# Optimization experiments

Hardware: AMD Instinct MI355X
Metric: run time of the kernel (lower is better)

## Reference

```python
import jax, jax.numpy as jnp
import numpy as np

NUM_CLASSES = 6
HIERARCHY_WEIGHT = 0.2


def _build_class_weights():
    w = np.ones(NUM_CLASSES, dtype=np.float32)
    w[0] = 1.2; w[1] = 1.0; w[2] = 1.1; w[3] = 1.3; w[4] = 1.0; w[5] = 1.1
    return jnp.asarray(w)


def _build_hierarchy_matrix():
    p = np.ones((NUM_CLASSES, NUM_CLASSES), dtype=np.float32)
    p[2, 3] = 0.5; p[3, 2] = 0.5
    p[0, 4] = 0.6; p[4, 0] = 0.6
    p[1, 5] = 0.7; p[5, 1] = 0.7
    p[0, 1] = 1.5; p[1, 0] = 1.5
    p[2, 5] = 1.4; p[5, 2] = 1.4
    return jnp.asarray(p)


def setup_inputs() -> dict:
    key = jax.random.key(0)
    k1, k2 = jax.random.split(key)
    B = 4194304
    predictions = jax.random.normal(k1, (B, NUM_CLASSES), dtype=jnp.float32)
    targets = jax.random.randint(k2, (B,), 0, NUM_CLASSES, dtype=jnp.int64)
    return {
        "predictions": predictions,
        "targets": targets,
        "class_weights": _build_class_weights(),
        "hierarchy_matrix": _build_hierarchy_matrix(),
    }


def reference(predictions, targets, class_weights, hierarchy_matrix):
    B = predictions.shape[0]
    # Weighted cross-entropy, matching torch's weighted-mean reduction:
    # sum_i w[t_i] * nll_i / sum_i w[t_i]
    logp = jax.nn.log_softmax(predictions, axis=-1)            # (B, C)
    nll = -jnp.take_along_axis(logp, targets[:, None], axis=-1)[:, 0]  # (B,)
    w = class_weights[targets]                                  # (B,)
    ce_loss = jnp.sum(w * nll) / jnp.sum(w)

    # Hierarchy penalty: sum_{i, j != t_i} probs[i,j] * penalty[t_i, j] / B
    probs = jax.nn.softmax(predictions, axis=-1)               # (B, C)
    pen = hierarchy_matrix[targets]                             # (B, C) gather of penalty rows
    not_target = 1.0 - jax.nn.one_hot(targets, NUM_CLASSES, dtype=probs.dtype)
    hierarchy_loss = jnp.sum(probs * pen * not_target) / B

    total_loss = ce_loss + HIERARCHY_WEIGHT * hierarchy_loss
    return total_loss, ce_loss, hierarchy_loss
```

## Files before the change

kernel.cpp:

```cpp
#include <hip/hip_runtime.h>

#define NC 6
constexpr float HIER_W = 0.2f;

__global__ __launch_bounds__(256) void hloss_main(
    const float* __restrict__ preds,
    const int*   __restrict__ targets,
    const float* __restrict__ cw,
    const float* __restrict__ pen,
    float4* __restrict__ partial,
    int nquads)
{
    __shared__ float s_cw[NC];
    __shared__ float s_pen[NC * NC];
    if (threadIdx.x < NC * NC) s_pen[threadIdx.x] = pen[threadIdx.x];
    if (threadIdx.x < NC)      s_cw[threadIdx.x]  = cw[threadIdx.x];
    __syncthreads();

    float a_num = 0.f, a_den = 0.f, a_h = 0.f;

    const int stride = gridDim.x * blockDim.x;
    for (int q = blockIdx.x * blockDim.x + threadIdx.x; q < nquads; q += stride) {
        const float4* base = reinterpret_cast<const float4*>(preds) + (size_t)q * 6;
        float4 v0 = base[0];
        float4 v1 = base[1];
        float4 v2 = base[2];
        float4 v3 = base[3];
        float4 v4 = base[4];
        float4 v5 = base[5];
        int4 t4 = reinterpret_cast<const int4*>(targets)[q];

        float x[24] = { v0.x, v0.y, v0.z, v0.w,  v1.x, v1.y, v1.z, v1.w,
                        v2.x, v2.y, v2.z, v2.w,  v3.x, v3.y, v3.z, v3.w,
                        v4.x, v4.y, v4.z, v4.w,  v5.x, v5.y, v5.z, v5.w };

        #pragma unroll
        for (int r = 0; r < 4; ++r) {
            const int tr = (r == 0) ? t4.x : (r == 1) ? t4.y : (r == 2) ? t4.z : t4.w;

            float e[NC], s = 0.f;
            #pragma unroll
            for (int j = 0; j < NC; ++j) { e[j] = __expf(x[r*NC + j]); s += e[j]; }
            const float inv = __frcp_rn(s);

            float xt = x[r*NC + 0];
            #pragma unroll
            for (int j = 1; j < NC; ++j) xt = (tr == j) ? x[r*NC + j] : xt;

            const float w   = s_cw[tr];
            const float nll = __logf(s) - xt;
            a_num += w * nll;
            a_den += w;

            const float* pr = s_pen + tr * NC;
            float dot = 0.f;
            #pragma unroll
            for (int j = 0; j < NC; ++j) dot += e[j] * pr[j];
            const float et = __expf(xt);
            a_h += (dot - et) * inv;
        }
    }

    #pragma unroll
    for (int off = 32; off > 0; off >>= 1) {
        a_num += __shfl_xor(a_num, off);
        a_den += __shfl_xor(a_den, off);
        a_h   += __shfl_xor(a_h,   off);
    }

    __shared__ float red[3][4];
    const int wave = threadIdx.x >> 6;
    const int lane = threadIdx.x & 63;
    if (lane == 0) { red[0][wave] = a_num; red[1][wave] = a_den; red[2][wave] = a_h; }
    __syncthreads();
    if (threadIdx.x == 0) {
        float n = 0.f, d = 0.f, h = 0.f;
        #pragma unroll
        for (int i = 0; i < 4; ++i) { n += red[0][i]; d += red[1][i]; h += red[2][i]; }
        partial[blockIdx.x] = make_float4(n, d, h, 0.f);
    }
}

__global__ __launch_bounds__(256) void hloss_reduce(
    const float4* __restrict__ partial, int nblocks,
    float* __restrict__ out, float invB)
{
    float n = 0.f, d = 0.f, h = 0.f;
    for (int i = threadIdx.x; i < nblocks; i += 256) {
        float4 p = partial[i];
        n += p.x; d += p.y; h += p.z;
    }
    #pragma unroll
    for (int off = 32; off > 0; off >>= 1) {
        n += __shfl_xor(n, off);
        d += __shfl_xor(d, off);
        h += __shfl_xor(h, off);
    }
    __shared__ float red[3][4];
    const int wave = threadIdx.x >> 6;
    const int lane = threadIdx.x & 63;
    if (lane == 0) { red[0][wave] = n; red[1][wave] = d; red[2][wave] = h; }
    __syncthreads();
    if (threadIdx.x == 0) {
        float N = 0.f, D = 0.f, H = 0.f;
        #pragma unroll
        for (int i = 0; i < 4; ++i) { N += red[0][i]; D += red[1][i]; H += red[2][i]; }
        const float ce = N / D;
        const float hh = H * invB;
        out[0] = ce + HIER_W * hh;
        out[1] = ce;
        out[2] = hh;
    }
}

extern "C" void kernel_launch(void* const* d_in, const int* in_sizes, int n_in,
                              void* d_out, int out_size, void* d_ws, size_t ws_size,
                              hipStream_t stream)
{
    const float* preds   = (const float*)d_in[0];
    const int*   targets = (const int*)  d_in[1];
    const float* cw      = (const float*)d_in[2];
    const float* pen     = (const float*)d_in[3];
    float4* partial = (float4*)d_ws;
    float* out = (float*)d_out;

    const int B = in_sizes[1];
    const int nquads = B / 4;

    const int threads = 256;
    const int blocks = 2048;

    hipLaunchKernelGGL(hloss_main, dim3(blocks), dim3(threads), 0, stream,
                       preds, targets, cw, pen, partial, nquads);
    hipLaunchKernelGGL(hloss_reduce, dim3(1), dim3(threads), 0, stream,
                       partial, blocks, out, 1.0f / (float)B);
}
```

Baseline: 30.65 us.

## Stage predictions and targets into LDS via async global_load_lds with double buffering

Replaces the grid-stride per-thread float4 loads with per-wave double-buffered asynchronous global-to-LDS copies (global_load_lds). Each wave handles 8 chunks of 128 rows, waiting on vmcnt so the next chunk's load overlaps compute on the current one. The grid now scales with B (B/4096 blocks, 1024 for the test size) instead of a fixed 2048. The aim is better memory-level parallelism and coalescing. It adds LDS traffic and hand-written waitcnt assumptions, and it requires B to be a multiple of 4096.

```diff
diff --git a/kernel.cpp b/kernel.cpp
--- a/kernel.cpp
+++ b/kernel.cpp
@@ -2,62 +2,96 @@
 
 #define NC 6
 constexpr float HIER_W = 0.2f;
+
+#define AS1 __attribute__((address_space(1)))
+#define AS3 __attribute__((address_space(3)))
+
+#define NITER 8
+#define STAGE_WORDS (128 * 6 + 128)
 
 __global__ __launch_bounds__(256) void hloss_main(
     const float* __restrict__ preds,
     const int*   __restrict__ targets,
     const float* __restrict__ cw,
     const float* __restrict__ pen,
-    float4* __restrict__ partial,
-    int nquads)
+    float4* __restrict__ partial)
 {
     __shared__ float s_cw[NC];
     __shared__ float s_pen[NC * NC];
+    __shared__ float s_stage[4][2][STAGE_WORDS];
+
     if (threadIdx.x < NC * NC) s_pen[threadIdx.x] = pen[threadIdx.x];
     if (threadIdx.x < NC)      s_cw[threadIdx.x]  = cw[threadIdx.x];
     __syncthreads();
 
+    const int wv   = threadIdx.x >> 6;
+    const int lane = threadIdx.x & 63;
+    const long long wrow0 = ((long long)blockIdx.x * 4 + wv) * (NITER * 128);
+
+    float* const st0 = &s_stage[wv][0][0];
+    float* const st1 = &s_stage[wv][1][0];
+
+    auto STAGE = [&](float* buf, int it) {
+        const long long r0 = wrow0 + (long long)it * 128;
+        const float* gp = preds + r0 * NC;
+        #pragma unroll
+        for (int k = 0; k < 3; ++k) {
+            __builtin_amdgcn_global_load_lds(
+                (const AS1 void*)(gp + k * 256 + lane * 4),
+                (AS3 void*)(buf + k * 256), 16, 0, 0);
+        }
+        const int* gt = targets + r0;
+        #pragma unroll
+        for (int k = 0; k < 2; ++k) {
+            __builtin_amdgcn_global_load_lds(
+                (const AS1 void*)(gt + k * 64 + lane),
+                (AS3 void*)(buf + 768 + k * 64), 4, 0, 0);
+        }
+    };
+
     float a_num = 0.f, a_den = 0.f, a_h = 0.f;
 
-    const int stride = gridDim.x * blockDim.x;
-    for (int q = blockIdx.x * blockDim.x + threadIdx.x; q < nquads; q += stride) {
-        const float4* base = reinterpret_cast<const float4*>(preds) + (size_t)q * 6;
-        float4 v0 = base[0];
-        float4 v1 = base[1];
-        float4 v2 = base[2];
-        float4 v3 = base[3];
-        float4 v4 = base[4];
-        float4 v5 = base[5];
-        int4 t4 = reinterpret_cast<const int4*>(targets)[q];
+    auto ROW = [&](const float* buf, int rr) {
+        const int tr = __float_as_int(buf[768 + rr]);
+        float xr[NC], e[NC], s = 0.f;
+        #pragma unroll
+        for (int j = 0; j < NC; ++j) xr[j] = buf[rr * 6 + j];
+        #pragma unroll
+        for (int j = 0; j < NC; ++j) { e[j] = __expf(xr[j]); s += e[j]; }
+        const float inv = __frcp_rn(s);
 
-        float x[24] = { v0.x, v0.y, v0.z, v0.w,  v1.x, v1.y, v1.z, v1.w,
-                        v2.x, v2.y, v2.z, v2.w,  v3.x, v3.y, v3.z, v3.w,
-                        v4.x, v4.y, v4.z, v4.w,  v5.x, v5.y, v5.z, v5.w };
+        float xt = xr[0];
+        #pragma unroll
+        for (int j = 1; j < NC; ++j) xt = (tr == j) ? xr[j] : xt;
 
+        const float w = s_cw[tr];
+        a_num += w * (__logf(s) - xt);
+        a_den += w;
+
+        const float* pr = s_pen + tr * NC;
+        float dot = 0.f;
         #pragma unroll
-        for (int r = 0; r < 4; ++r) {
-            const int tr = (r == 0) ? t4.x : (r == 1) ? t4.y : (r == 2) ? t4.z : t4.w;
+        for (int j = 0; j < NC; ++j) dot += e[j] * pr[j];
+        a_h += (dot - __expf(xt)) * inv;
+    };
 
-            float e[NC], s = 0.f;
-            #pragma unroll
-            for (int j = 0; j < NC; ++j) { e[j] = __expf(x[r*NC + j]); s += e[j]; }
-            const float inv = __frcp_rn(s);
+    STAGE(st0, 0);
+    STAGE(st1, 1);
 
-            float xt = x[r*NC + 0];
-            #pragma unroll
-            for (int j = 1; j < NC; ++j) xt = (tr == j) ? x[r*NC + j] : xt;
+    #pragma unroll
+    for (int it = 0; it < NITER; ++it) {
+        float* buf = (it & 1) ? st1 : st0;
+        if (it < NITER - 1) { asm volatile("s_waitcnt vmcnt(5)" ::: "memory"); }
+        else                { asm volatile("s_waitcnt vmcnt(0)" ::: "memory"); }
+        __builtin_amdgcn_sched_barrier(0);
 
-            const float w   = s_cw[tr];
-            const float nll = __logf(s) - xt;
-            a_num += w * nll;
-            a_den += w;
+        ROW(buf, lane);
+        ROW(buf, 64 + lane);
 
-            const float* pr = s_pen + tr * NC;
-            float dot = 0.f;
-            #pragma unroll
-            for (int j = 0; j < NC; ++j) dot += e[j] * pr[j];
-            const float et = __expf(xt);
-            a_h += (dot - et) * inv;
+        if (it + 2 < NITER) {
+            asm volatile("s_waitcnt lgkmcnt(0)" ::: "memory");
+            __builtin_amdgcn_sched_barrier(0);
+            STAGE(buf, it + 2);
         }
     }
 
@@ -69,9 +103,7 @@
     }
 
     __shared__ float red[3][4];
-    const int wave = threadIdx.x >> 6;
-    const int lane = threadIdx.x & 63;
-    if (lane == 0) { red[0][wave] = a_num; red[1][wave] = a_den; red[2][wave] = a_h; }
+    if (lane == 0) { red[0][wv] = a_num; red[1][wv] = a_den; red[2][wv] = a_h; }
     __syncthreads();
     if (threadIdx.x == 0) {
         float n = 0.f, d = 0.f, h = 0.f;
@@ -125,13 +157,10 @@
     float* out = (float*)d_out;
 
     const int B = in_sizes[1];
-    const int nquads = B / 4;
+    const int blocks = B / 4096;
 
-    const int threads = 256;
-    const int blocks = 2048;
-
-    hipLaunchKernelGGL(hloss_main, dim3(blocks), dim3(threads), 0, stream,
-                       preds, targets, cw, pen, partial, nquads);
-    hipLaunchKernelGGL(hloss_reduce, dim3(1), dim3(threads), 0, stream,
+    hipLaunchKernelGGL(hloss_main, dim3(blocks), dim3(256), 0, stream,
+                       preds, targets, cw, pen, partial);
+    hipLaunchKernelGGL(hloss_reduce, dim3(1), dim3(256), 0, stream,
                        partial, blocks, out, 1.0f / (float)B);
 }
```

Result: faster. 27.32 us (-10.9%).
